# Kernel tuning notes

Hardware: AMD Instinct MI355X
Metric: run time of the kernel (lower is better)

## Reference

```python
import jax, jax.numpy as jnp
import numpy as np

LEVEL = 256
GROUPS = 1
SHIFT = (LEVEL - 1) / 2.0  # symmetric affine shift folded from quant.shift buffer


def qdq(x, clip_val, level=LEVEL, groups=GROUPS, shift=SHIFT):
    """Per-group clip + level quantize-dequantize (what custom_quant.Quant saves/restores).
    clip_val: [groups]. Group split is over equal contiguous chunks of the flattened tensor."""
    shp = x.shape
    xg = x.reshape(groups, -1)
    scale = (2.0 * clip_val) / (level - 1)          # [groups]
    scale = scale.reshape(groups, 1)
    q = jnp.clip(jnp.round(xg / scale + shift), 0.0, level - 1.0)
    return ((q - shift) * scale).reshape(shp)


def setup_inputs() -> dict:
    key = jax.random.key(0)
    k1, k2 = jax.random.split(key)
    # attention-style batched matmul: [B,H,S,Dh] @ [B,H,Dh,S]
    x1 = jax.random.normal(k1, (2, 12, 1024, 64), dtype=jnp.float32)
    x2 = jax.random.normal(k2, (2, 12, 64, 1024), dtype=jnp.float32)
    clip_val1 = 2.0 * jnp.ones((GROUPS,), dtype=jnp.float32)
    clip_val2 = 2.0 * jnp.ones((GROUPS,), dtype=jnp.float32)
    return {"x1": x1, "x2": x2, "clip_val1": clip_val1, "clip_val2": clip_val2}


def reference(x1, x2, clip_val1, clip_val2):
    # Faithful to matmul.forward: the quantized copies are only SAVED for backward;
    # the forward output itself is computed on the full-precision operands.
    # (qdq is exercised in the fwdbwd reference.)
    return jnp.matmul(x1, x2)  # [2,12,1024,1024]
```

## Files before the change

kernel.cpp:

```cpp
#include <hip/hip_runtime.h>
#include <hip/hip_bf16.h>


#define NN 1024
#define KK 64

typedef __attribute__((ext_vector_type(4))) float  float4v;
typedef __attribute__((ext_vector_type(8))) short  bf16x8;
typedef __attribute__((ext_vector_type(16))) float floatx16;

__device__ __forceinline__ short f2bs(float f) {
    union { float f; unsigned u; } in;
    in.f = f;
    unsigned u = in.u;
    return (short)((u + 0x7FFFu + ((u >> 16) & 1u)) >> 16);
}


__global__ __launch_bounds__(256) void reformat_A(const float* __restrict__ A,
                                                  short* __restrict__ Aw) {
    int t0 = blockIdx.x * 256 + threadIdx.x;
    #pragma unroll
    for (int it = 0; it < 4; ++it) {
        int task = t0 + it * 49152;
        int bh   = task >> 13;
        int rem  = task & 8191;
        int m    = rem >> 3;
        int kg   = rem & 7;
        const float4v* p = (const float4v*)(A + (size_t)task * 8);
        float4v v0 = p[0];
        float4v v1 = p[1];
        int ks = kg >> 1, q = kg & 1;
        int mt = m >> 5;
        int lane = (m & 31) + (q << 5);
        size_t dst = ((size_t)((bh * 32 + mt) * 4 + ks)) * 512 + (size_t)lane * 8;
        bf16x8 o;
        o[0] = f2bs(v0.x); o[1] = f2bs(v0.y); o[2] = f2bs(v0.z); o[3] = f2bs(v0.w);
        o[4] = f2bs(v1.x); o[5] = f2bs(v1.y); o[6] = f2bs(v1.z); o[7] = f2bs(v1.w);
        *(bf16x8*)(Aw + dst) = o;
    }
}

__global__ __launch_bounds__(256) void reformat_B(const float* __restrict__ B,
                                                  short* __restrict__ Bw) {
    int t0 = blockIdx.x * 256 + threadIdx.x;
    #pragma unroll
    for (int it = 0; it < 4; ++it) {
        int task = t0 + it * 49152;
        int kg   = task / 24576;
        int rem  = task - kg * 24576;
        int bh   = rem >> 10;
        int n    = rem & 1023;
        const float* p = B + (size_t)bh * 65536 + (size_t)kg * 8192 + n;
        float v0 = p[0 * 1024], v1 = p[1 * 1024], v2 = p[2 * 1024], v3 = p[3 * 1024];
        float v4 = p[4 * 1024], v5 = p[5 * 1024], v6 = p[6 * 1024], v7 = p[7 * 1024];
        int ks = kg >> 1, q = kg & 1;
        int nt = n >> 5;
        int lane = (n & 31) + (q << 5);
        size_t dst = ((size_t)((bh * 32 + nt) * 4 + ks)) * 512 + (size_t)lane * 8;
        bf16x8 o;
        o[0] = f2bs(v0); o[1] = f2bs(v1); o[2] = f2bs(v2); o[3] = f2bs(v3);
        o[4] = f2bs(v4); o[5] = f2bs(v5); o[6] = f2bs(v6); o[7] = f2bs(v7);
        *(bf16x8*)(Bw + dst) = o;
    }
}

__global__ __launch_bounds__(256) void bmm_frag(const short* __restrict__ Aw,
                                                const short* __restrict__ Bw,
                                                float* __restrict__ C) {
    const int tid  = threadIdx.x;
    const int lane = tid & 63;
    const int w    = tid >> 6;
    const int bx = blockIdx.x;
    const int by = blockIdx.y;
    const int bh = blockIdx.z;
    const int wm = (w >> 1) * 2;
    const int wn = (w & 1) * 2;

    const short* Ab = Aw + ((size_t)((bh * 32 + by * 4 + wm) * 4)) * 512 + (size_t)lane * 8;
    const short* Bb = Bw + ((size_t)((bh * 32 + bx * 4 + wn) * 4)) * 512 + (size_t)lane * 8;

    floatx16 acc[2][2];
    #pragma unroll
    for (int mi = 0; mi < 2; ++mi)
        #pragma unroll
        for (int ni = 0; ni < 2; ++ni)
            #pragma unroll
            for (int r = 0; r < 16; ++r)
                acc[mi][ni][r] = 0.0f;

    #pragma unroll
    for (int ks = 0; ks < 4; ++ks) {
        bf16x8 a0 = *(const bf16x8*)(Ab + ks * 512);
        bf16x8 a1 = *(const bf16x8*)(Ab + 2048 + ks * 512);
        bf16x8 b0 = *(const bf16x8*)(Bb + ks * 512);
        bf16x8 b1 = *(const bf16x8*)(Bb + 2048 + ks * 512);
        acc[0][0] = __builtin_amdgcn_mfma_f32_32x32x16_bf16(b0, a0, acc[0][0], 0, 0, 0);
        acc[0][1] = __builtin_amdgcn_mfma_f32_32x32x16_bf16(b1, a0, acc[0][1], 0, 0, 0);
        acc[1][0] = __builtin_amdgcn_mfma_f32_32x32x16_bf16(b0, a1, acc[1][0], 0, 0, 0);
        acc[1][1] = __builtin_amdgcn_mfma_f32_32x32x16_bf16(b1, a1, acc[1][1], 0, 0, 0);
    }

    const int mc = lane & 31;
    const int nb = (lane >> 5) * 4;
    float* Cb = C + ((size_t)bh << 20)
                  + (size_t)(by * 128 + wm * 32 + mc) * NN
                  + bx * 128 + wn * 32 + nb;

    #pragma unroll
    for (int mi = 0; mi < 2; ++mi) {
        #pragma unroll
        for (int ni = 0; ni < 2; ++ni) {
            float* Ct = Cb + (size_t)(mi * 32) * NN + ni * 32;
            #pragma unroll
            for (int g = 0; g < 4; ++g) {
                float4v o;
                o.x = acc[mi][ni][4 * g + 0];
                o.y = acc[mi][ni][4 * g + 1];
                o.z = acc[mi][ni][4 * g + 2];
                o.w = acc[mi][ni][4 * g + 3];
                *(float4v*)(Ct + 8 * g) = o;
            }
        }
    }
}

extern "C" void kernel_launch(void* const* d_in, const int* in_sizes, int n_in,
                              void* d_out, int out_size, void* d_ws, size_t ws_size,
                              hipStream_t stream) {
    const float* x1 = (const float*)d_in[0];
    const float* x2 = (const float*)d_in[1];
    float* out = (float*)d_out;

    short* Aw = (short*)d_ws;
    short* Bw = Aw + 1572864;

    hipLaunchKernelGGL(reformat_A, dim3(192), dim3(256), 0, stream, x1, Aw);
    hipLaunchKernelGGL(reformat_B, dim3(192), dim3(256), 0, stream, x2, Bw);
    hipLaunchKernelGGL(bmm_frag, dim3(8, 8, 24), dim3(256), 0, stream, Aw, Bw, out);
}
```

Before: 127.8 us.

## Merge reformat kernels and store C with nontemporal per-lane coalesced writes

```diff
diff --git a/kernel.cpp b/kernel.cpp
--- a/kernel.cpp
+++ b/kernel.cpp
@@ -17,51 +17,52 @@
 }
 
 
-__global__ __launch_bounds__(256) void reformat_A(const float* __restrict__ A,
-                                                  short* __restrict__ Aw) {
-    int t0 = blockIdx.x * 256 + threadIdx.x;
-    #pragma unroll
-    for (int it = 0; it < 4; ++it) {
-        int task = t0 + it * 49152;
-        int bh   = task >> 13;
-        int rem  = task & 8191;
-        int m    = rem >> 3;
-        int kg   = rem & 7;
-        const float4v* p = (const float4v*)(A + (size_t)task * 8);
-        float4v v0 = p[0];
-        float4v v1 = p[1];
-        int ks = kg >> 1, q = kg & 1;
-        int mt = m >> 5;
-        int lane = (m & 31) + (q << 5);
-        size_t dst = ((size_t)((bh * 32 + mt) * 4 + ks)) * 512 + (size_t)lane * 8;
-        bf16x8 o;
-        o[0] = f2bs(v0.x); o[1] = f2bs(v0.y); o[2] = f2bs(v0.z); o[3] = f2bs(v0.w);
-        o[4] = f2bs(v1.x); o[5] = f2bs(v1.y); o[6] = f2bs(v1.z); o[7] = f2bs(v1.w);
-        *(bf16x8*)(Aw + dst) = o;
-    }
-}
-
-__global__ __launch_bounds__(256) void reformat_B(const float* __restrict__ B,
-                                                  short* __restrict__ Bw) {
-    int t0 = blockIdx.x * 256 + threadIdx.x;
-    #pragma unroll
-    for (int it = 0; it < 4; ++it) {
-        int task = t0 + it * 49152;
-        int kg   = task / 24576;
-        int rem  = task - kg * 24576;
-        int bh   = rem >> 10;
-        int n    = rem & 1023;
-        const float* p = B + (size_t)bh * 65536 + (size_t)kg * 8192 + n;
-        float v0 = p[0 * 1024], v1 = p[1 * 1024], v2 = p[2 * 1024], v3 = p[3 * 1024];
-        float v4 = p[4 * 1024], v5 = p[5 * 1024], v6 = p[6 * 1024], v7 = p[7 * 1024];
-        int ks = kg >> 1, q = kg & 1;
-        int nt = n >> 5;
-        int lane = (n & 31) + (q << 5);
-        size_t dst = ((size_t)((bh * 32 + nt) * 4 + ks)) * 512 + (size_t)lane * 8;
-        bf16x8 o;
-        o[0] = f2bs(v0); o[1] = f2bs(v1); o[2] = f2bs(v2); o[3] = f2bs(v3);
-        o[4] = f2bs(v4); o[5] = f2bs(v5); o[6] = f2bs(v6); o[7] = f2bs(v7);
-        *(bf16x8*)(Bw + dst) = o;
+__global__ __launch_bounds__(256) void reformat_AB(const float* __restrict__ A,
+                                                   const float* __restrict__ B,
+                                                   short* __restrict__ Aw,
+                                                   short* __restrict__ Bw) {
+    if (blockIdx.x < 192) {
+        int t0 = blockIdx.x * 256 + threadIdx.x;
+        #pragma unroll
+        for (int it = 0; it < 4; ++it) {
+            int task = t0 + it * 49152;
+            int bh   = task >> 13;
+            int rem  = task & 8191;
+            int m    = rem >> 3;
+            int kg   = rem & 7;
+            const float4v* p = (const float4v*)(A + (size_t)task * 8);
+            float4v v0 = p[0];
+            float4v v1 = p[1];
+            int ks = kg >> 1, q = kg & 1;
+            int mt = m >> 5;
+            int lane = (m & 31) + (q << 5);
+            size_t dst = ((size_t)((bh * 32 + mt) * 4 + ks)) * 512 + (size_t)lane * 8;
+            bf16x8 o;
+            o[0] = f2bs(v0.x); o[1] = f2bs(v0.y); o[2] = f2bs(v0.z); o[3] = f2bs(v0.w);
+            o[4] = f2bs(v1.x); o[5] = f2bs(v1.y); o[6] = f2bs(v1.z); o[7] = f2bs(v1.w);
+            *(bf16x8*)(Aw + dst) = o;
+        }
+    } else {
+        int t0 = (blockIdx.x - 192) * 256 + threadIdx.x;
+        #pragma unroll
+        for (int it = 0; it < 4; ++it) {
+            int task = t0 + it * 49152;
+            int kg   = task / 24576;
+            int rem  = task - kg * 24576;
+            int bh   = rem >> 10;
+            int n    = rem & 1023;
+            const float* p = B + (size_t)bh * 65536 + (size_t)kg * 8192 + n;
+            float v0 = p[0 * 1024], v1 = p[1 * 1024], v2 = p[2 * 1024], v3 = p[3 * 1024];
+            float v4 = p[4 * 1024], v5 = p[5 * 1024], v6 = p[6 * 1024], v7 = p[7 * 1024];
+            int ks = kg >> 1, q = kg & 1;
+            int nt = n >> 5;
+            int lane = (n & 31) + (q << 5);
+            size_t dst = ((size_t)((bh * 32 + nt) * 4 + ks)) * 512 + (size_t)lane * 8;
+            bf16x8 o;
+            o[0] = f2bs(v0); o[1] = f2bs(v1); o[2] = f2bs(v2); o[3] = f2bs(v3);
+            o[4] = f2bs(v4); o[5] = f2bs(v5); o[6] = f2bs(v6); o[7] = f2bs(v7);
+            *(bf16x8*)(Bw + dst) = o;
+        }
     }
 }
 
@@ -95,17 +96,17 @@
         bf16x8 a1 = *(const bf16x8*)(Ab + 2048 + ks * 512);
         bf16x8 b0 = *(const bf16x8*)(Bb + ks * 512);
         bf16x8 b1 = *(const bf16x8*)(Bb + 2048 + ks * 512);
-        acc[0][0] = __builtin_amdgcn_mfma_f32_32x32x16_bf16(b0, a0, acc[0][0], 0, 0, 0);
-        acc[0][1] = __builtin_amdgcn_mfma_f32_32x32x16_bf16(b1, a0, acc[0][1], 0, 0, 0);
-        acc[1][0] = __builtin_amdgcn_mfma_f32_32x32x16_bf16(b0, a1, acc[1][0], 0, 0, 0);
-        acc[1][1] = __builtin_amdgcn_mfma_f32_32x32x16_bf16(b1, a1, acc[1][1], 0, 0, 0);
+        acc[0][0] = __builtin_amdgcn_mfma_f32_32x32x16_bf16(a0, b0, acc[0][0], 0, 0, 0);
+        acc[0][1] = __builtin_amdgcn_mfma_f32_32x32x16_bf16(a0, b1, acc[0][1], 0, 0, 0);
+        acc[1][0] = __builtin_amdgcn_mfma_f32_32x32x16_bf16(a1, b0, acc[1][0], 0, 0, 0);
+        acc[1][1] = __builtin_amdgcn_mfma_f32_32x32x16_bf16(a1, b1, acc[1][1], 0, 0, 0);
     }
 
-    const int mc = lane & 31;
-    const int nb = (lane >> 5) * 4;
+    const int nc    = lane & 31;
+    const int rbase = (lane >> 5) * 4;
     float* Cb = C + ((size_t)bh << 20)
-                  + (size_t)(by * 128 + wm * 32 + mc) * NN
-                  + bx * 128 + wn * 32 + nb;
+                  + (size_t)(by * 128 + wm * 32) * NN
+                  + bx * 128 + wn * 32 + nc;
 
     #pragma unroll
     for (int mi = 0; mi < 2; ++mi) {
@@ -113,13 +114,9 @@
         for (int ni = 0; ni < 2; ++ni) {
             float* Ct = Cb + (size_t)(mi * 32) * NN + ni * 32;
             #pragma unroll
-            for (int g = 0; g < 4; ++g) {
-                float4v o;
-                o.x = acc[mi][ni][4 * g + 0];
-                o.y = acc[mi][ni][4 * g + 1];
-                o.z = acc[mi][ni][4 * g + 2];
-                o.w = acc[mi][ni][4 * g + 3];
-                *(float4v*)(Ct + 8 * g) = o;
+            for (int r = 0; r < 16; ++r) {
+                int row = rbase + (r & 3) + ((r >> 2) * 8);
+                __builtin_nontemporal_store(acc[mi][ni][r], Ct + (size_t)row * NN);
             }
         }
     }
@@ -135,7 +132,6 @@
     short* Aw = (short*)d_ws;
     short* Bw = Aw + 1572864;
 
-    hipLaunchKernelGGL(reformat_A, dim3(192), dim3(256), 0, stream, x1, Aw);
-    hipLaunchKernelGGL(reformat_B, dim3(192), dim3(256), 0, stream, x2, Bw);
+    hipLaunchKernelGGL(reformat_AB, dim3(384), dim3(256), 0, stream, x1, x2, Aw, Bw);
     hipLaunchKernelGGL(bmm_frag, dim3(8, 8, 24), dim3(256), 0, stream, Aw, Bw, out);
 }
```

After: 123.3 us. -3.5%, faster.
